# Performance work log

Measured on AMD Instinct MI355X. Metric: run time of the kernel, lower is better.

Reference implementation:

```python
import jax, jax.numpy as jnp
import numpy as np

N_NODES = 50000
HIDDEN = 128
N_EDGES = 600000
DROPOUT_RATE = 0.25


def setup_inputs() -> dict:
    key = jax.random.key(0)
    k_x, k_e, k_w1, k_w2 = jax.random.split(key, 4)
    x = jax.random.normal(k_x, (N_NODES, HIDDEN), dtype=jnp.float32)
    edge_index = jax.random.randint(k_e, (2, N_EDGES), 0, N_NODES, dtype=jnp.int64)
    # Linear layers: torch Linear default init ~ U(-1/sqrt(fan_in), 1/sqrt(fan_in))
    s = 1.0 / np.sqrt(HIDDEN)
    W1 = jax.random.uniform(k_w1, (HIDDEN, HIDDEN), jnp.float32, -s, s)
    b1 = jnp.zeros((HIDDEN,), jnp.float32)
    W2 = jax.random.uniform(k_w2, (HIDDEN, HIDDEN), jnp.float32, -s, s)
    b2 = jnp.zeros((HIDDEN,), jnp.float32)
    return {"x": x, "edge_index": edge_index, "W1": W1, "b1": b1, "W2": W2, "b2": b2}


def reference(x, edge_index, W1, b1, W2, b2):
    # Feature-dim dropout mask (bernoulli over hidden dim, broadcast over nodes).
    mask_key = jax.random.key(42)
    mask = jax.random.bernoulli(mask_key, 1.0 - DROPOUT_RATE, (x.shape[1],)).astype(x.dtype)
    xd = x * mask[None, :]  # [N, D]

    # GINConv aggregation: sum of source-node features at destination nodes.
    src, dst = edge_index[0], edge_index[1]
    agg = jax.ops.segment_sum(xd[src], dst, num_segments=x.shape[0])  # [N, D]

    # (1 + eps) * x + agg, eps = 0 (GINConv default)
    h = xd + agg

    # 2-layer MLP: Linear -> ReLU -> Linear
    h = jax.nn.relu(h @ W1 + b1)
    out = h @ W2 + b2
    return out
```

## Files before the change

kernel.cpp:

```cpp
#include <hip/hip_runtime.h>

#define N_NODES 50000
#define HIDDEN  128
#define N_EDGES 600000
#define BR      32
#define NB      ((N_NODES + 255) / 256)
#define NTILES  ((N_NODES + BR - 1) / BR)
#define E_PAD_MAX (N_EDGES + 3 * N_NODES)
#define SCSR_CAP 4096

typedef __attribute__((ext_vector_type(8))) short short8v;
typedef __attribute__((ext_vector_type(4))) float f32x4;

__device__ __forceinline__ unsigned rotl32(unsigned v, int r) {
  return (v << r) | (v >> (32 - r));
}

__device__ __forceinline__ void threefry2x32(unsigned x0, unsigned x1,
                                             unsigned& o0, unsigned& o1) {
  const unsigned ks0 = 0u, ks1 = 42u;
  const unsigned ks2 = ks0 ^ ks1 ^ 0x1BD11BDAu;
  const unsigned ks[3] = {ks0, ks1, ks2};
  const int rot[2][4] = {{13, 15, 26, 6}, {17, 29, 16, 24}};
  x0 += ks0; x1 += ks1;
#pragma unroll
  for (int i = 0; i < 5; ++i) {
#pragma unroll
    for (int j = 0; j < 4; ++j) {
      x0 += x1;
      x1 = rotl32(x1, rot[i & 1][j]);
      x1 ^= x0;
    }
    x0 += ks[(i + 1) % 3];
    x1 += ks[(i + 2) % 3] + (unsigned)(i + 1);
  }
  o0 = x0; o1 = x1;
}

__device__ __forceinline__ float col_mask(int c) {
  unsigned o0, o1;
  threefry2x32(0u, (unsigned)c, o0, o1);
  unsigned bits = o0 ^ o1;
  float u = __uint_as_float((bits >> 9) | 0x3f800000u) - 1.0f;
  return (u < 0.75f) ? 1.0f : 0.0f;
}

__device__ __forceinline__ unsigned short f2bf(float f) {
  unsigned u = __float_as_uint(f);
  u += 0x7fffu + ((u >> 16) & 1u);
  return (unsigned short)(u >> 16);
}

__device__ __forceinline__ float bflo(unsigned u) {
  return __uint_as_float(u << 16);
}
__device__ __forceinline__ float bfhi(unsigned u) {
  return __uint_as_float(u & 0xffff0000u);
}

__device__ __forceinline__ float rlane(float v, int l) {
  return __int_as_float(__builtin_amdgcn_readlane(__float_as_int(v), l));
}

__global__ __launch_bounds__(256) void prep_kernel(
    const float* __restrict__ x, const float* __restrict__ W1,
    const float* __restrict__ W2, const int* __restrict__ ei,
    unsigned short* __restrict__ xb, unsigned short* __restrict__ Wt1,
    unsigned short* __restrict__ Wt2, int* __restrict__ deg) {
  __shared__ float msk[HIDDEN];
  if (threadIdx.x < HIDDEN) msk[threadIdx.x] = col_mask(threadIdx.x);
  __syncthreads();

  const int gid = blockIdx.x * 256 + threadIdx.x;
  const int e0 = gid * 8;
  if (e0 < N_NODES * HIDDEN) {
    const int c0 = e0 & (HIDDEN - 1);
    const float4 v0 = *reinterpret_cast<const float4*>(x + e0);
    const float4 v1 = *reinterpret_cast<const float4*>(x + e0 + 4);
    unsigned short h[8];
    h[0] = f2bf(v0.x * msk[c0 + 0]);
    h[1] = f2bf(v0.y * msk[c0 + 1]);
    h[2] = f2bf(v0.z * msk[c0 + 2]);
    h[3] = f2bf(v0.w * msk[c0 + 3]);
    h[4] = f2bf(v1.x * msk[c0 + 4]);
    h[5] = f2bf(v1.y * msk[c0 + 5]);
    h[6] = f2bf(v1.z * msk[c0 + 6]);
    h[7] = f2bf(v1.w * msk[c0 + 7]);
    *reinterpret_cast<uint4*>(xb + e0) = *reinterpret_cast<uint4*>(h);
  }
  if (gid < N_EDGES) atomicAdd(deg + ei[N_EDGES + gid], 1);
  if (gid < HIDDEN * HIDDEN / 4) {
#pragma unroll
    for (int i = 0; i < 4; ++i) {
      int t = gid * 4 + i;
      int col = t >> 7, k = t & 127;
      Wt1[t] = f2bf(W1[k * HIDDEN + col]);
      Wt2[t] = f2bf(W2[k * HIDDEN + col]);
    }
  }
  if (gid < 16) {
    uint4 z; z.x = 0; z.y = 0; z.z = 0; z.w = 0;
    *reinterpret_cast<uint4*>(xb + (size_t)N_NODES * HIDDEN + gid * 8) = z;
  }
}

__global__ __launch_bounds__(256) void scanA_kernel(const int* __restrict__ deg,
                                                    int* __restrict__ bsum) {
  int idx = blockIdx.x * 256 + threadIdx.x;
  int v = (idx < N_NODES) ? ((deg[idx] + 3) & ~3) : 0;
#pragma unroll
  for (int off = 32; off; off >>= 1) v += __shfl_down(v, off, 64);
  __shared__ int ws4[4];
  if ((threadIdx.x & 63) == 0) ws4[threadIdx.x >> 6] = v;
  __syncthreads();
  if (threadIdx.x == 0) bsum[blockIdx.x] = ws4[0] + ws4[1] + ws4[2] + ws4[3];
}

__global__ __launch_bounds__(256) void scanB_kernel(const int* __restrict__ bsum,
                                                    int* __restrict__ bpre,
                                                    int* __restrict__ offs) {
  __shared__ int s[256];
  const int t = threadIdx.x;
  int v = (t < NB) ? bsum[t] : 0;
  s[t] = v;
  __syncthreads();
  int acc = v;
  for (int off = 1; off < 256; off <<= 1) {
    int add = (t >= off) ? s[t - off] : 0;
    __syncthreads();
    acc += add;
    s[t] = acc;
    __syncthreads();
  }
  if (t < NB) bpre[t] = acc - v;
  if (t == 0) offs[N_NODES] = s[255];
}

__global__ __launch_bounds__(256) void scanC_kernel(
    const int* __restrict__ deg, const int* __restrict__ bpre,
    int* __restrict__ offs, int* __restrict__ pos,
    unsigned short* __restrict__ csr) {
  __shared__ int s[256];
  const int t = threadIdx.x;
  const int idx = blockIdx.x * 256 + t;
  int d = (idx < N_NODES) ? deg[idx] : 0;
  int v = (d + 3) & ~3;
  s[t] = v;
  __syncthreads();
  int acc = v;
  for (int off = 1; off < 256; off <<= 1) {
    int add = (t >= off) ? s[t - off] : 0;
    __syncthreads();
    acc += add;
    s[t] = acc;
    __syncthreads();
  }
  if (idx < N_NODES) {
    int o = bpre[blockIdx.x] + acc - v;
    offs[idx] = o;
    pos[idx] = o;
    for (int w = o + d; w < o + v; ++w)
      csr[w] = (unsigned short)N_NODES;
  }
}

__global__ __launch_bounds__(256) void fill_kernel(const int* __restrict__ ei,
                                                   int* __restrict__ pos,
                                                   unsigned short* __restrict__ csr) {
  int e = blockIdx.x * blockDim.x + threadIdx.x;
  if (e >= N_EDGES) return;
  int src = ei[e];
  int dst = ei[N_EDGES + e];
  int p = atomicAdd(pos + dst, 1);
  csr[p] = (unsigned short)src;
}

template <bool LDSIDX>
__device__ __forceinline__ void gather2(
    int base, int wave, int q, int ql, int cs,
    const unsigned short* __restrict__ csr, const unsigned short* scsr,
    const int* loffs, const unsigned short* __restrict__ xb,
    unsigned short* H1) {
#pragma unroll 1
  for (int i = 0; i < 2; ++i) {
    const int row = wave * 8 + i * 4 + q;
    const int node = base + row;
    const bool valid = node < N_NODES;
    const int s = valid ? loffs[row] : 0;
    const int e = valid ? loffs[row + 1] : 0;
    const int on = valid ? node : N_NODES;
    const uint4 ov =
        *reinterpret_cast<const uint4*>(xb + (size_t)on * HIDDEN + ql * 8);
    float a0 = bflo(ov.x), a1 = bfhi(ov.x);
    float a2 = bflo(ov.y), a3 = bfhi(ov.y);
    float a4 = bflo(ov.z), a5 = bfhi(ov.z);
    float a6 = bflo(ov.w), a7 = bfhi(ov.w);

    const bool h0 = s < e;
    uint2 pk;
    pk.x = 0; pk.y = 0;
    if (h0)
      pk = LDSIDX ? *reinterpret_cast<const uint2*>(scsr + (s - cs))
                  : *reinterpret_cast<const uint2*>(csr + s);
    int i0 = h0 ? (int)(pk.x & 0xffffu) : N_NODES;
    int i1 = h0 ? (int)(pk.x >> 16) : N_NODES;
    int i2 = h0 ? (int)(pk.y & 0xffffu) : N_NODES;
    int i3 = h0 ? (int)(pk.y >> 16) : N_NODES;
    uint4 c0 = *reinterpret_cast<const uint4*>(xb + (size_t)i0 * HIDDEN + ql * 8);
    uint4 c1 = *reinterpret_cast<const uint4*>(xb + (size_t)i1 * HIDDEN + ql * 8);
    uint4 c2 = *reinterpret_cast<const uint4*>(xb + (size_t)i2 * HIDDEN + ql * 8);
    uint4 c3 = *reinterpret_cast<const uint4*>(xb + (size_t)i3 * HIDDEN + ql * 8);

    for (int j = s; j < e; j += 4) {
      const int jn = j + 4;
      const bool more = jn < e;
      uint2 pk2;
      pk2.x = 0; pk2.y = 0;
      if (more)
        pk2 = LDSIDX ? *reinterpret_cast<const uint2*>(scsr + (jn - cs))
                     : *reinterpret_cast<const uint2*>(csr + jn);
      const int n0 = more ? (int)(pk2.x & 0xffffu) : N_NODES;
      const int n1 = more ? (int)(pk2.x >> 16) : N_NODES;
      const int n2 = more ? (int)(pk2.y & 0xffffu) : N_NODES;
      const int n3 = more ? (int)(pk2.y >> 16) : N_NODES;
      const uint4 d0 =
          *reinterpret_cast<const uint4*>(xb + (size_t)n0 * HIDDEN + ql * 8);
      const uint4 d1 =
          *reinterpret_cast<const uint4*>(xb + (size_t)n1 * HIDDEN + ql * 8);
      const uint4 d2 =
          *reinterpret_cast<const uint4*>(xb + (size_t)n2 * HIDDEN + ql * 8);
      const uint4 d3 =
          *reinterpret_cast<const uint4*>(xb + (size_t)n3 * HIDDEN + ql * 8);

      a0 += bflo(c0.x) + bflo(c1.x) + bflo(c2.x) + bflo(c3.x);
      a1 += bfhi(c0.x) + bfhi(c1.x) + bfhi(c2.x) + bfhi(c3.x);
      a2 += bflo(c0.y) + bflo(c1.y) + bflo(c2.y) + bflo(c3.y);
      a3 += bfhi(c0.y) + bfhi(c1.y) + bfhi(c2.y) + bfhi(c3.y);
      a4 += bflo(c0.z) + bflo(c1.z) + bflo(c2.z) + bflo(c3.z);
      a5 += bfhi(c0.z) + bfhi(c1.z) + bfhi(c2.z) + bfhi(c3.z);
      a6 += bflo(c0.w) + bflo(c1.w) + bflo(c2.w) + bflo(c3.w);
      a7 += bfhi(c0.w) + bfhi(c1.w) + bfhi(c2.w) + bfhi(c3.w);

      c0 = d0; c1 = d1; c2 = d2; c3 = d3;
    }
    uint4 pw;
    pw.x = (unsigned)f2bf(a0) | ((unsigned)f2bf(a1) << 16);
    pw.y = (unsigned)f2bf(a2) | ((unsigned)f2bf(a3) << 16);
    pw.z = (unsigned)f2bf(a4) | ((unsigned)f2bf(a5) << 16);
    pw.w = (unsigned)f2bf(a6) | ((unsigned)f2bf(a7) << 16);
    const int byte = (row * 256 + ql * 16) ^ ((row & 7) << 4);
    *reinterpret_cast<uint4*>(reinterpret_cast<char*>(H1) + byte) = pw;
  }
}

__global__ __launch_bounds__(256) void fused_xb_kernel(
    const int* __restrict__ offs, const unsigned short* __restrict__ csr,
    const unsigned short* __restrict__ xb,
    const unsigned short* __restrict__ Wt1,
    const unsigned short* __restrict__ Wt2, const float* __restrict__ b1,
    const float* __restrict__ b2, float* __restrict__ out) {
  __shared__ unsigned short H1[BR * HIDDEN];
  __shared__ unsigned short H2[BR * HIDDEN];
  __shared__ __align__(16) unsigned short scsr[SCSR_CAP];
  __shared__ int loffs[BR + 1];

  const int tid = threadIdx.x;
  const int lane = tid & 63;
  const int wave = tid >> 6;
  const int base = blockIdx.x * BR;

  if (tid < BR + 1) {
    int idx = base + tid;
    loffs[tid] = offs[idx > N_NODES ? N_NODES : idx];
  }
  __syncthreads();
  const int cs = loffs[0];
  const int count = loffs[BR] - cs;
  const bool stage = (count <= SCSR_CAP);
  if (stage) {
    const unsigned* src = reinterpret_cast<const unsigned*>(csr + cs);
    unsigned* dst = reinterpret_cast<unsigned*>(scsr);
    for (int k = tid; k < (count >> 1); k += 256) dst[k] = src[k];
  }
  __syncthreads();

  const int q = lane >> 4;
  const int ql = lane & 15;

  if (stage)
    gather2<true>(base, wave, q, ql, cs, csr, scsr, loffs, xb, H1);
  else
    gather2<false>(base, wave, q, ql, cs, csr, scsr, loffs, xb, H1);
  __syncthreads();

  const int colbase = wave * 32;
  float bias1[2], bias2[2];
#pragma unroll
  for (int c = 0; c < 2; ++c) {
    bias1[c] = b1[colbase + c * 16 + (lane & 15)];
    bias2[c] = b2[colbase + c * 16 + (lane & 15)];
  }

  f32x4 acc[2][2] = {};
#pragma unroll
  for (int kt = 0; kt < 4; ++kt) {
    short8v a[2], b[2];
#pragma unroll
    for (int r = 0; r < 2; ++r) {
      int row = r * 16 + (lane & 15);
      int byte = (row * 256 + kt * 64 + (lane >> 4) * 16) ^ ((row & 7) << 4);
      a[r] = *reinterpret_cast<const short8v*>(
          reinterpret_cast<const char*>(H1) + byte);
    }
#pragma unroll
    for (int c = 0; c < 2; ++c) {
      int col = colbase + c * 16 + (lane & 15);
      b[c] = *reinterpret_cast<const short8v*>(
          reinterpret_cast<const char*>(Wt1) + col * 256 + kt * 64 +
          (lane >> 4) * 16);
    }
#pragma unroll
    for (int r = 0; r < 2; ++r)
#pragma unroll
      for (int c = 0; c < 2; ++c)
        acc[r][c] = __builtin_amdgcn_mfma_f32_16x16x32_bf16(a[r], b[c],
                                                            acc[r][c], 0, 0, 0);
  }
#pragma unroll
  for (int r = 0; r < 2; ++r)
#pragma unroll
    for (int c = 0; c < 2; ++c)
#pragma unroll
      for (int q2 = 0; q2 < 4; ++q2) {
        int row = r * 16 + (lane >> 4) * 4 + q2;
        int col = colbase + c * 16 + (lane & 15);
        float v = fmaxf(acc[r][c][q2] + bias1[c], 0.f);
        int byte = (row * 256 + col * 2) ^ ((row & 7) << 4);
        *reinterpret_cast<unsigned short*>(reinterpret_cast<char*>(H2) + byte) =
            f2bf(v);
      }
  __syncthreads();

  f32x4 acc2[2][2] = {};
#pragma unroll
  for (int kt = 0; kt < 4; ++kt) {
    short8v a[2], b[2];
#pragma unroll
    for (int r = 0; r < 2; ++r) {
      int row = r * 16 + (lane & 15);
      int byte = (row * 256 + kt * 64 + (lane >> 4) * 16) ^ ((row & 7) << 4);
      a[r] = *reinterpret_cast<const short8v*>(
          reinterpret_cast<const char*>(H2) + byte);
    }
#pragma unroll
    for (int c = 0; c < 2; ++c) {
      int col = colbase + c * 16 + (lane & 15);
      b[c] = *reinterpret_cast<const short8v*>(
          reinterpret_cast<const char*>(Wt2) + col * 256 + kt * 64 +
          (lane >> 4) * 16);
    }
#pragma unroll
    for (int r = 0; r < 2; ++r)
#pragma unroll
      for (int c = 0; c < 2; ++c)
        acc2[r][c] = __builtin_amdgcn_mfma_f32_16x16x32_bf16(
            a[r], b[c], acc2[r][c], 0, 0, 0);
  }
#pragma unroll
  for (int r = 0; r < 2; ++r)
#pragma unroll
    for (int c = 0; c < 2; ++c)
#pragma unroll
      for (int q2 = 0; q2 < 4; ++q2) {
        int row = base + r * 16 + (lane >> 4) * 4 + q2;
        if (row < N_NODES) {
          int col = colbase + c * 16 + (lane & 15);
          out[(size_t)row * HIDDEN + col] = acc2[r][c][q2] + bias2[c];
        }
      }
}

__global__ __launch_bounds__(256) void scatter_kernel(
    const int* __restrict__ ei, const float* __restrict__ x,
    float* __restrict__ agg) {
  long long gid = (long long)blockIdx.x * blockDim.x + threadIdx.x;
  int e = (int)(gid >> 5);
  if (e >= N_EDGES) return;
  int sub = ((int)gid & 31) * 4;
  int src = ei[e];
  int dst = ei[N_EDGES + e];
  const float4 v = *reinterpret_cast<const float4*>(x + src * HIDDEN + sub);
  float* p = agg + dst * HIDDEN + sub;
  atomicAdd(p + 0, v.x);
  atomicAdd(p + 1, v.y);
  atomicAdd(p + 2, v.z);
  atomicAdd(p + 3, v.w);
}

__global__ __launch_bounds__(512) void mlp_kernel(
    const float* __restrict__ x, float* __restrict__ io,
    const float* __restrict__ W1, const float* __restrict__ b1,
    const float* __restrict__ W2, const float* __restrict__ b2) {
  __shared__ float W1s[HIDDEN * HIDDEN];
  __shared__ float W2s[HIDDEN * HIDDEN];

  const int tid = threadIdx.x;
#pragma unroll
  for (int i = 0; i < 8; ++i) {
    int idx = (i * 512 + tid) * 4;
    *reinterpret_cast<float4*>(W1s + idx) =
        *reinterpret_cast<const float4*>(W1 + idx);
    *reinterpret_cast<float4*>(W2s + idx) =
        *reinterpret_cast<const float4*>(W2 + idx);
  }

  const int lane = tid & 63;
  const int wave = tid >> 6;
  const int c0 = 2 * lane, c1 = 2 * lane + 1;

  const float m0 = col_mask(c0);
  const float m1 = col_mask(c1);
  const float bb1x = b1[c0], bb1y = b1[c1];
  const float bb2x = b2[c0], bb2y = b2[c1];

  __syncthreads();

  const int gwave = blockIdx.x * 8 + wave;
  const int nwaves = gridDim.x * 8;

  for (int pr = gwave; pr < N_NODES / 2; pr += nwaves) {
    const int baseA = (2 * pr) * HIDDEN;
    const int baseB = baseA + HIDDEN;

    float2 xA = *reinterpret_cast<const float2*>(x + baseA + c0);
    float2 gA = *reinterpret_cast<const float2*>(io + baseA + c0);
    float2 xB = *reinterpret_cast<const float2*>(x + baseB + c0);
    float2 gB = *reinterpret_cast<const float2*>(io + baseB + c0);

    float hA0 = m0 * (xA.x + gA.x), hA1 = m1 * (xA.y + gA.y);
    float hB0 = m0 * (xB.x + gB.x), hB1 = m1 * (xB.y + gB.y);

    float aA0 = bb1x, aA1 = bb1y, aB0 = bb1x, aB1 = bb1y;
#pragma unroll
    for (int k = 0; k < HIDDEN; ++k) {
      const int sl = k >> 1;
      float hkA = (k & 1) ? rlane(hA1, sl) : rlane(hA0, sl);
      float hkB = (k & 1) ? rlane(hB1, sl) : rlane(hB0, sl);
      float2 w = *reinterpret_cast<const float2*>(W1s + k * HIDDEN + c0);
      aA0 = fmaf(hkA, w.x, aA0);
      aA1 = fmaf(hkA, w.y, aA1);
      aB0 = fmaf(hkB, w.x, aB0);
      aB1 = fmaf(hkB, w.y, aB1);
    }
    aA0 = fmaxf(aA0, 0.0f); aA1 = fmaxf(aA1, 0.0f);
    aB0 = fmaxf(aB0, 0.0f); aB1 = fmaxf(aB1, 0.0f);

    float oA0 = bb2x, oA1 = bb2y, oB0 = bb2x, oB1 = bb2y;
#pragma unroll
    for (int k = 0; k < HIDDEN; ++k) {
      const int sl = k >> 1;
      float hkA = (k & 1) ? rlane(aA1, sl) : rlane(aA0, sl);
      float hkB = (k & 1) ? rlane(aB1, sl) : rlane(aB0, sl);
      float2 w = *reinterpret_cast<const float2*>(W2s + k * HIDDEN + c0);
      oA0 = fmaf(hkA, w.x, oA0);
      oA1 = fmaf(hkA, w.y, oA1);
      oB0 = fmaf(hkB, w.x, oB0);
      oB1 = fmaf(hkB, w.y, oB1);
    }

    *reinterpret_cast<float2*>(io + baseA + c0) = make_float2(oA0, oA1);
    *reinterpret_cast<float2*>(io + baseB + c0) = make_float2(oB0, oB1);
  }
}

extern "C" void kernel_launch(void* const* d_in, const int* in_sizes, int n_in,
                              void* d_out, int out_size, void* d_ws,
                              size_t ws_size, hipStream_t stream) {
  (void)in_sizes; (void)n_in; (void)out_size;
  const float* x  = (const float*)d_in[0];
  const int*   ei = (const int*)d_in[1];
  const float* W1 = (const float*)d_in[2];
  const float* b1 = (const float*)d_in[3];
  const float* W2 = (const float*)d_in[4];
  const float* b2 = (const float*)d_in[5];
  float* out = (float*)d_out;

  const size_t int_words = (size_t)N_NODES + (N_NODES + 1) + N_NODES + 2 * NB;
  const size_t int_pad   = (int_words * 4 + 15) & ~(size_t)15;
  const size_t csr_bytes = (size_t)E_PAD_MAX * 2;
  const size_t wt_bytes  = 2 * (size_t)HIDDEN * HIDDEN * 2;
  const size_t xb_bytes  = (size_t)(N_NODES + 1) * HIDDEN * 2;
  const size_t need = int_pad + csr_bytes + wt_bytes + xb_bytes;

  if (ws_size >= need) {
    char* wsb = (char*)d_ws;
    int* deg  = (int*)wsb;
    int* offs = deg + N_NODES;
    int* pos  = offs + N_NODES + 1;
    int* bsum = pos + N_NODES;
    int* bpre = bsum + NB;
    unsigned short* csr = (unsigned short*)(wsb + int_pad);
    unsigned short* Wt1 = (unsigned short*)(wsb + int_pad + csr_bytes);
    unsigned short* Wt2 = Wt1 + HIDDEN * HIDDEN;
    unsigned short* xb  = Wt2 + HIDDEN * HIDDEN;

    hipMemsetAsync(deg, 0, (size_t)N_NODES * 4, stream);
    const int nprep = (N_NODES * HIDDEN / 8 + 255) / 256;
    prep_kernel<<<nprep, 256, 0, stream>>>(x, W1, W2, ei, xb, Wt1, Wt2, deg);
    scanA_kernel<<<NB, 256, 0, stream>>>(deg, bsum);
    scanB_kernel<<<1, 256, 0, stream>>>(bsum, bpre, offs);
    scanC_kernel<<<NB, 256, 0, stream>>>(deg, bpre, offs, pos, csr);
    fill_kernel<<<(N_EDGES + 255) / 256, 256, 0, stream>>>(ei, pos, csr);
    fused_xb_kernel<<<NTILES, 256, 0, stream>>>(offs, csr, xb, Wt1, Wt2, b1,
                                                b2, out);
  } else {
    hipMemsetAsync(out, 0, (size_t)N_NODES * HIDDEN * sizeof(float), stream);
    const long long total = (long long)N_EDGES * 32;
    scatter_kernel<<<(int)((total + 255) / 256), 256, 0, stream>>>(ei, x, out);
    mlp_kernel<<<256, 512, 0, stream>>>(x, out, W1, b1, W2, b2);
  }
}
```

Measured before the change: 117.7 us.

## Fold block-scan into scanC, replace memset with init kernel, pair edges in fill

The single-block scanB launch is removed: every scanC block now redundantly scans the block sums in LDS to get its own prefix. The hipMemsetAsync of the degree array is replaced by an init kernel that also does the weight transpose/bf16 conversion and zero-row setup previously done in prep. fill_kernel now handles two edges per thread with int2 loads. This aims to cut launch count and serial small-kernel latency, at the cost of redundant scan work per block.

```diff
diff --git a/kernel.cpp b/kernel.cpp
--- a/kernel.cpp
+++ b/kernel.cpp
@@ -62,11 +62,30 @@
   return __int_as_float(__builtin_amdgcn_readlane(__float_as_int(v), l));
 }
 
+__global__ __launch_bounds__(256) void init_kernel(
+    const float* __restrict__ W1, const float* __restrict__ W2,
+    unsigned short* __restrict__ Wt1, unsigned short* __restrict__ Wt2,
+    int* __restrict__ deg, unsigned short* __restrict__ xb) {
+  const int gid = blockIdx.x * 256 + threadIdx.x;
+  if (gid < N_NODES) deg[gid] = 0;
+  if (gid < HIDDEN * HIDDEN / 4) {
+#pragma unroll
+    for (int i = 0; i < 4; ++i) {
+      int t = gid * 4 + i;
+      int col = t >> 7, k = t & 127;
+      Wt1[t] = f2bf(W1[k * HIDDEN + col]);
+      Wt2[t] = f2bf(W2[k * HIDDEN + col]);
+    }
+  }
+  if (gid < 16) {
+    uint4 z; z.x = 0; z.y = 0; z.z = 0; z.w = 0;
+    *reinterpret_cast<uint4*>(xb + (size_t)N_NODES * HIDDEN + gid * 8) = z;
+  }
+}
+
 __global__ __launch_bounds__(256) void prep_kernel(
-    const float* __restrict__ x, const float* __restrict__ W1,
-    const float* __restrict__ W2, const int* __restrict__ ei,
-    unsigned short* __restrict__ xb, unsigned short* __restrict__ Wt1,
-    unsigned short* __restrict__ Wt2, int* __restrict__ deg) {
+    const float* __restrict__ x, const int* __restrict__ ei,
+    unsigned short* __restrict__ xb, int* __restrict__ deg) {
   __shared__ float msk[HIDDEN];
   if (threadIdx.x < HIDDEN) msk[threadIdx.x] = col_mask(threadIdx.x);
   __syncthreads();
@@ -89,19 +108,6 @@
     *reinterpret_cast<uint4*>(xb + e0) = *reinterpret_cast<uint4*>(h);
   }
   if (gid < N_EDGES) atomicAdd(deg + ei[N_EDGES + gid], 1);
-  if (gid < HIDDEN * HIDDEN / 4) {
-#pragma unroll
-    for (int i = 0; i < 4; ++i) {
-      int t = gid * 4 + i;
-      int col = t >> 7, k = t & 127;
-      Wt1[t] = f2bf(W1[k * HIDDEN + col]);
-      Wt2[t] = f2bf(W2[k * HIDDEN + col]);
-    }
-  }
-  if (gid < 16) {
-    uint4 z; z.x = 0; z.y = 0; z.z = 0; z.w = 0;
-    *reinterpret_cast<uint4*>(xb + (size_t)N_NODES * HIDDEN + gid * 8) = z;
-  }
 }
 
 __global__ __launch_bounds__(256) void scanA_kernel(const int* __restrict__ deg,
@@ -116,12 +122,32 @@
   if (threadIdx.x == 0) bsum[blockIdx.x] = ws4[0] + ws4[1] + ws4[2] + ws4[3];
 }
 
-__global__ __launch_bounds__(256) void scanB_kernel(const int* __restrict__ bsum,
-                                                    int* __restrict__ bpre,
-                                                    int* __restrict__ offs) {
+__global__ __launch_bounds__(256) void scanC_kernel(
+    const int* __restrict__ deg, const int* __restrict__ bsum,
+    int* __restrict__ offs, int* __restrict__ pos,
+    unsigned short* __restrict__ csr) {
+  __shared__ int sb[256];
   __shared__ int s[256];
   const int t = threadIdx.x;
-  int v = (t < NB) ? bsum[t] : 0;
+  const int b = blockIdx.x;
+
+  int bv = (t < NB) ? bsum[t] : 0;
+  sb[t] = bv;
+  __syncthreads();
+  int bacc = bv;
+  for (int off = 1; off < 256; off <<= 1) {
+    int add = (t >= off) ? sb[t - off] : 0;
+    __syncthreads();
+    bacc += add;
+    sb[t] = bacc;
+    __syncthreads();
+  }
+  const int bpre = (b > 0) ? sb[b - 1] : 0;
+  if (b == NB - 1 && t == 0) offs[N_NODES] = sb[NB - 1];
+
+  const int idx = b * 256 + t;
+  int d = (idx < N_NODES) ? deg[idx] : 0;
+  int v = (d + 3) & ~3;
   s[t] = v;
   __syncthreads();
   int acc = v;
@@ -132,31 +158,8 @@
     s[t] = acc;
     __syncthreads();
   }
-  if (t < NB) bpre[t] = acc - v;
-  if (t == 0) offs[N_NODES] = s[255];
-}
-
-__global__ __launch_bounds__(256) void scanC_kernel(
-    const int* __restrict__ deg, const int* __restrict__ bpre,
-    int* __restrict__ offs, int* __restrict__ pos,
-    unsigned short* __restrict__ csr) {
-  __shared__ int s[256];
-  const int t = threadIdx.x;
-  const int idx = blockIdx.x * 256 + t;
-  int d = (idx < N_NODES) ? deg[idx] : 0;
-  int v = (d + 3) & ~3;
-  s[t] = v;
-  __syncthreads();
-  int acc = v;
-  for (int off = 1; off < 256; off <<= 1) {
-    int add = (t >= off) ? s[t - off] : 0;
-    __syncthreads();
-    acc += add;
-    s[t] = acc;
-    __syncthreads();
-  }
   if (idx < N_NODES) {
-    int o = bpre[blockIdx.x] + acc - v;
+    int o = bpre + acc - v;
     offs[idx] = o;
     pos[idx] = o;
     for (int w = o + d; w < o + v; ++w)
@@ -167,12 +170,14 @@
 __global__ __launch_bounds__(256) void fill_kernel(const int* __restrict__ ei,
                                                    int* __restrict__ pos,
                                                    unsigned short* __restrict__ csr) {
-  int e = blockIdx.x * blockDim.x + threadIdx.x;
-  if (e >= N_EDGES) return;
-  int src = ei[e];
-  int dst = ei[N_EDGES + e];
-  int p = atomicAdd(pos + dst, 1);
-  csr[p] = (unsigned short)src;
+  int e0 = (blockIdx.x * 256 + threadIdx.x) * 2;
+  if (e0 >= N_EDGES) return;
+  const int2 src2 = *reinterpret_cast<const int2*>(ei + e0);
+  const int2 dst2 = *reinterpret_cast<const int2*>(ei + N_EDGES + e0);
+  int p0 = atomicAdd(pos + dst2.x, 1);
+  csr[p0] = (unsigned short)src2.x;
+  int p1 = atomicAdd(pos + dst2.y, 1);
+  csr[p1] = (unsigned short)src2.y;
 }
 
 template <bool LDSIDX>
@@ -485,7 +490,7 @@
   const float* b2 = (const float*)d_in[5];
   float* out = (float*)d_out;
 
-  const size_t int_words = (size_t)N_NODES + (N_NODES + 1) + N_NODES + 2 * NB;
+  const size_t int_words = (size_t)N_NODES + (N_NODES + 1) + N_NODES + NB;
   const size_t int_pad   = (int_words * 4 + 15) & ~(size_t)15;
   const size_t csr_bytes = (size_t)E_PAD_MAX * 2;
   const size_t wt_bytes  = 2 * (size_t)HIDDEN * HIDDEN * 2;
@@ -498,19 +503,17 @@
     int* offs = deg + N_NODES;
     int* pos  = offs + N_NODES + 1;
     int* bsum = pos + N_NODES;
-    int* bpre = bsum + NB;
     unsigned short* csr = (unsigned short*)(wsb + int_pad);
     unsigned short* Wt1 = (unsigned short*)(wsb + int_pad + csr_bytes);
     unsigned short* Wt2 = Wt1 + HIDDEN * HIDDEN;
     unsigned short* xb  = Wt2 + HIDDEN * HIDDEN;
 
-    hipMemsetAsync(deg, 0, (size_t)N_NODES * 4, stream);
+    init_kernel<<<NB, 256, 0, stream>>>(W1, W2, Wt1, Wt2, deg, xb);
     const int nprep = (N_NODES * HIDDEN / 8 + 255) / 256;
-    prep_kernel<<<nprep, 256, 0, stream>>>(x, W1, W2, ei, xb, Wt1, Wt2, deg);
+    prep_kernel<<<nprep, 256, 0, stream>>>(x, ei, xb, deg);
     scanA_kernel<<<NB, 256, 0, stream>>>(deg, bsum);
-    scanB_kernel<<<1, 256, 0, stream>>>(bsum, bpre, offs);
-    scanC_kernel<<<NB, 256, 0, stream>>>(deg, bpre, offs, pos, csr);
-    fill_kernel<<<(N_EDGES + 255) / 256, 256, 0, stream>>>(ei, pos, csr);
+    scanC_kernel<<<NB, 256, 0, stream>>>(deg, bsum, offs, pos, csr);
+    fill_kernel<<<(N_EDGES / 2 + 255) / 256, 256, 0, stream>>>(ei, pos, csr);
     fused_xb_kernel<<<NTILES, 256, 0, stream>>>(offs, csr, xb, Wt1, Wt2, b1,
                                                 b2, out);
   } else {
```

New measurement: 116.9 us. Within noise of the previous version (-0.6%).
